# Optimization experiments

Measured on AMD Instinct MI355X. Metric: run time of the kernel, lower is better.

Reference implementation:

```python
import jax, jax.numpy as jnp
import numpy as np

T, B, H = 1024, 4096, 4  # time steps, students, BKT params (l,f,g,s)


def setup_inputs() -> dict:
    key = jax.random.key(0)
    ks = jax.random.split(key, 6)
    # binary correctness sequences, like the original BKT data
    x = (jax.random.uniform(ks[0], (T, B, 1)) < 0.5).astype(jnp.float32)
    y = (jax.random.uniform(ks[1], (T, B, 1)) < 0.5).astype(jnp.float32)
    s = 1.0 / np.sqrt(H)  # torch nn.RNN default init: U(-1/sqrt(H), 1/sqrt(H))
    W_ih = jax.random.uniform(ks[2], (H, 1), minval=-s, maxval=s, dtype=jnp.float32)
    W_hh = jax.random.uniform(ks[3], (H, H), minval=-s, maxval=s, dtype=jnp.float32)
    b_ih = jax.random.uniform(ks[4], (H,), minval=-s, maxval=s, dtype=jnp.float32)
    b_hh = jax.random.uniform(ks[5], (H,), minval=-s, maxval=s, dtype=jnp.float32)
    prior = jnp.array([0.1], dtype=jnp.float32)
    return {"x": x, "y": y, "prior": prior, "W_ih": W_ih, "W_hh": W_hh,
            "b_ih": b_ih, "b_hh": b_hh}


def _bce(p, y):
    # torch BCELoss clamps log terms at -100
    logp = jnp.maximum(jnp.log(p), -100.0)
    log1mp = jnp.maximum(jnp.log(1.0 - p), -100.0)
    return -(y * logp + (1.0 - y) * log1mp).mean()


def _forward(x, y, prior, W_ih, W_hh, b_ih, b_hh):
    Bn = x.shape[1]
    Hn = W_hh.shape[0]

    # --- Elman RNN (tanh), seq-first, h0 = 0 ---
    def rnn_step(h, x_t):  # x_t: [B,1], h: [B,H]
        h = jnp.tanh(x_t @ W_ih.T + b_ih + h @ W_hh.T + b_hh)
        return h, h

    h0 = jnp.zeros((Bn, Hn), dtype=x.dtype)
    _, output = jax.lax.scan(rnn_step, h0, x)  # [T,B,H]
    params = (output + 1.0) / 2.0  # map tanh output into (0,1)

    # --- sequential nonlinear BKT latent recurrence ---
    latent0 = jnp.broadcast_to(jax.nn.sigmoid(prior), (Bn, 1)).astype(x.dtype)

    def bkt_step(latent, inp):
        p_t, y_t = inp  # p_t: [B,H], y_t: [B,1]
        l, f, g, s = p_t[:, 0:1], p_t[:, 1:2], p_t[:, 2:3], p_t[:, 3:4]
        correct = latent * (1 - s) + (1 - latent) * g
        k_t1 = latent * (1 - s) / (latent * (1 - s) + (1 - latent) * g)
        k_t0 = latent * s / (latent * s + (1 - latent) * (1 - g))
        m_t = k_t1 * correct + k_t0 * (1 - correct)
        next_latent = m_t * (1 - f) + (1 - m_t) * l
        return next_latent, (correct, next_latent, _bce(correct, y_t))

    _, (corrects, latents, losses) = jax.lax.scan(bkt_step, latent0, (params, y))
    loss = losses.mean()  # sum of per-step BCE / T
    return corrects, latents, loss


def reference(x, y, prior, W_ih, W_hh, b_ih, b_hh):
    return _forward(x, y, prior, W_ih, W_hh, b_ih, b_hh)
```

## Files before the change

kernel.cpp:

```cpp
#include <hip/hip_runtime.h>

#define TT 1024
#define BB 4096
#define CHUNK 64
#define WARM 160
#define NCH (TT / CHUNK)
#define NWMAX 7

typedef float v2f __attribute__((ext_vector_type(2)));

__launch_bounds__(64, 1)
__global__ void bkt_rnn_k(const float* __restrict__ x,
                          const float* __restrict__ y,
                          const float* __restrict__ prior,
                          const float* __restrict__ W_ih,
                          const float* __restrict__ W_hh,
                          const float* __restrict__ b_ih,
                          const float* __restrict__ b_hh,
                          float* __restrict__ out,
                          float* __restrict__ lossPart)
{
    __shared__ unsigned xls[NWMAX * 64];

    const int lane = threadIdx.x;
    const int c  = blockIdx.x >> 6;
    const int eg = blockIdx.x & 63;
    const int e  = eg * 64 + lane;

    const int t_out0  = c * CHUNK;
    const int nwarm   = (t_out0 > WARM) ? WARM : t_out0;
    const int t_start = t_out0 - nwarm;
    const int nww     = nwarm >> 5;
    const int nwords  = nww + 2;

    const float* xp = x + (size_t)t_start * BB + e;
    for (int wd = 0; wd < nwords; ++wd) {
        unsigned m = 0;
        #pragma unroll
        for (int i = 0; i < 32; ++i)
            if (xp[(size_t)(wd * 32 + i) * BB] != 0.0f) m |= (1u << i);
        xls[wd * 64 + lane] = m;
    }
    const float* ypb = y + (size_t)t_out0 * BB + e;
    unsigned yw0 = 0, yw1 = 0;
    #pragma unroll
    for (int i = 0; i < 32; ++i) {
        if (ypb[(size_t)i * BB] != 0.0f)        yw0 |= (1u << i);
        if (ypb[(size_t)(i + 32) * BB] != 0.0f) yw1 |= (1u << i);
    }

    const float S = 2.8853900817779268f;
    float basev[4], swv[4], vv[4][4];
    #pragma unroll
    for (int jj = 0; jj < 4; ++jj) {
        float rowsum = W_hh[jj * 4 + 0] + W_hh[jj * 4 + 1] + W_hh[jj * 4 + 2] + W_hh[jj * 4 + 3];
        basev[jj] = S * (b_ih[jj] + b_hh[jj] + rowsum);
        swv[jj]   = S * W_ih[jj];
        #pragma unroll
        for (int kk = 0; kk < 4; ++kk) vv[jj][kk] = -2.f * S * W_hh[jj * 4 + kk];
    }
    const v2f base01 = {basev[0], basev[1]}, base23 = {basev[2], basev[3]};
    const v2f sw01   = {swv[0],   swv[1]},   sw23   = {swv[2],   swv[3]};
    const v2f c0_01 = {vv[0][0], vv[1][0]}, c0_23 = {vv[2][0], vv[3][0]};
    const v2f c1_01 = {vv[0][1], vv[1][1]}, c1_23 = {vv[2][1], vv[3][1]};
    const v2f c2_01 = {vv[0][2], vv[1][2]}, c2_23 = {vv[2][2], vv[3][2]};
    const v2f c3_01 = {vv[0][3], vv[1][3]}, c3_23 = {vv[2][3], vv[3][3]};

    float lat = 1.0f / (1.0f + __builtin_amdgcn_exp2f(-1.4426950408889634f * prior[0]));
    float r0 = 0.5f, r1 = 0.5f, r2 = 0.5f, r3 = 0.5f;
    float lossAcc = 0.0f;

    auto step = [&](float xf) {
        v2f xv  = {xf, xf};
        v2f r0b = {r0, r0}, r1b = {r1, r1}, r2b = {r2, r2}, r3b = {r3, r3};
        v2f z01 = __builtin_elementwise_fma(xv, sw01, base01);
        v2f z23 = __builtin_elementwise_fma(xv, sw23, base23);
        z01 = __builtin_elementwise_fma(r0b, c0_01, z01);
        z23 = __builtin_elementwise_fma(r0b, c0_23, z23);
        z01 = __builtin_elementwise_fma(r1b, c1_01, z01);
        z23 = __builtin_elementwise_fma(r1b, c1_23, z23);
        z01 = __builtin_elementwise_fma(r2b, c2_01, z01);
        z23 = __builtin_elementwise_fma(r2b, c2_23, z23);
        z01 = __builtin_elementwise_fma(r3b, c3_01, z01);
        z23 = __builtin_elementwise_fma(r3b, c3_23, z23);
        r0 = __builtin_amdgcn_rcpf(__builtin_amdgcn_exp2f(z01.x) + 1.0f);
        r1 = __builtin_amdgcn_rcpf(__builtin_amdgcn_exp2f(z01.y) + 1.0f);
        r2 = __builtin_amdgcn_rcpf(__builtin_amdgcn_exp2f(z23.x) + 1.0f);
        r3 = __builtin_amdgcn_rcpf(__builtin_amdgcn_exp2f(z23.y) + 1.0f);
    };

    for (int wd = 0; wd < nww; ++wd) {
        unsigned m = xls[wd * 64 + lane];
        #pragma unroll 8
        for (int i = 0; i < 32; ++i) {
            step((float)((m >> i) & 1u));
            lat = fmaf(lat, (r0 + r1) - 1.0f, 1.0f - r0);
        }
    }

    unsigned mo0 = xls[nww * 64 + lane];
    unsigned mo1 = xls[(nww + 1) * 64 + lane];
    float* cO = out + (size_t)t_out0 * BB + e;
    float* lO = cO + (size_t)TT * BB;

    auto outblock = [&](unsigned mw, unsigned yw, int tb) {
        float prod = 1.0f;
        #pragma unroll 8
        for (int i = 0; i < 32; ++i) {
            step((float)((mw >> i) & 1u));
            float corr = fmaf(lat, (r2 + r3) - 1.0f, 1.0f - r2);
            float nl   = fmaf(lat, (r0 + r1) - 1.0f, 1.0f - r0);
            const size_t off = (size_t)(tb + i) * BB;
            cO[off] = corr;
            lO[off] = nl;
            float lp = ((yw >> i) & 1u) ? corr : (1.0f - corr);
            prod *= lp;
            if ((i & 7) == 7) {
                lossAcc += __builtin_amdgcn_logf(prod) * 0.6931471805599453f;
                prod = 1.0f;
            }
            lat = nl;
        }
    };
    outblock(mo0, yw0, 0);
    outblock(mo1, yw1, 32);

    #pragma unroll
    for (int o = 32; o >= 1; o >>= 1) lossAcc += __shfl_xor(lossAcc, o, 64);
    if (lane == 0) lossPart[blockIdx.x] = lossAcc;
}

__global__ void reduce_k(const float* __restrict__ part, float* __restrict__ loss) {
    float acc = 0.f;
    for (int i = threadIdx.x; i < 1024; i += 256) acc += part[i];
    #pragma unroll
    for (int o = 32; o >= 1; o >>= 1) acc += __shfl_xor(acc, o, 64);
    __shared__ float w[4];
    if ((threadIdx.x & 63) == 0) w[threadIdx.x >> 6] = acc;
    __syncthreads();
    if (threadIdx.x == 0) {
        float t = w[0] + w[1] + w[2] + w[3];
        *loss = t * (-1.0f / ((float)TT * (float)BB));
    }
}

extern "C" void kernel_launch(void* const* d_in, const int* in_sizes, int n_in,
                              void* d_out, int out_size, void* d_ws, size_t ws_size,
                              hipStream_t stream) {
    const float* x    = (const float*)d_in[0];
    const float* y    = (const float*)d_in[1];
    const float* pr   = (const float*)d_in[2];
    const float* W_ih = (const float*)d_in[3];
    const float* W_hh = (const float*)d_in[4];
    const float* b_ih = (const float*)d_in[5];
    const float* b_hh = (const float*)d_in[6];
    float* out = (float*)d_out;
    float* lossPart = (float*)d_ws;

    bkt_rnn_k<<<NCH * 64, 64, 0, stream>>>(x, y, pr, W_ih, W_hh, b_ih, b_hh, out, lossPart);
    reduce_k<<<1, 256, 0, stream>>>(lossPart, out + 2 * (size_t)TT * BB);
}
```

Baseline: 117.6 us.

## Split BKT recurrence into affine chunk scan with shorter RNN warmup

```diff
diff --git a/kernel.cpp b/kernel.cpp
--- a/kernel.cpp
+++ b/kernel.cpp
@@ -3,111 +3,216 @@
 #define TT 1024
 #define BB 4096
 #define CHUNK 64
-#define WARM 160
+#define WH 64
 #define NCH (TT / CHUNK)
-#define NWMAX 7
+#define NB  (NCH * BB)
+
+#define WS_A   1024
+#define WS_B   (WS_A + NB)
+#define WS_H   (WS_B + NB)
+#define WS_XW  (WS_H + 4 * NB)
 
 typedef float v2f __attribute__((ext_vector_type(2)));
 
+struct StepC {
+    v2f base01, base23, sw01, sw23;
+    v2f c0_01, c0_23, c1_01, c1_23, c2_01, c2_23, c3_01, c3_23;
+};
+
+__device__ __forceinline__ StepC make_consts(const float* W_ih, const float* W_hh,
+                                             const float* b_ih, const float* b_hh) {
+    const float S = 2.8853900817779268f;
+    float basev[4], swv[4], vv[4][4];
+    #pragma unroll
+    for (int jj = 0; jj < 4; ++jj) {
+        float rowsum = W_hh[jj*4+0] + W_hh[jj*4+1] + W_hh[jj*4+2] + W_hh[jj*4+3];
+        basev[jj] = S * (b_ih[jj] + b_hh[jj] + rowsum);
+        swv[jj]   = S * W_ih[jj];
+        #pragma unroll
+        for (int kk = 0; kk < 4; ++kk) vv[jj][kk] = -2.f * S * W_hh[jj*4+kk];
+    }
+    StepC K;
+    K.base01 = {basev[0], basev[1]}; K.base23 = {basev[2], basev[3]};
+    K.sw01   = {swv[0],   swv[1]};   K.sw23   = {swv[2],   swv[3]};
+    K.c0_01 = {vv[0][0], vv[1][0]};  K.c0_23 = {vv[2][0], vv[3][0]};
+    K.c1_01 = {vv[0][1], vv[1][1]};  K.c1_23 = {vv[2][1], vv[3][1]};
+    K.c2_01 = {vv[0][2], vv[1][2]};  K.c2_23 = {vv[2][2], vv[3][2]};
+    K.c3_01 = {vv[0][3], vv[1][3]};  K.c3_23 = {vv[2][3], vv[3][3]};
+    return K;
+}
+
+__device__ __forceinline__ void rnn_step(const StepC& K, float xf,
+                                         float& r0, float& r1, float& r2, float& r3) {
+    v2f xv  = {xf, xf};
+    v2f r0b = {r0, r0}, r1b = {r1, r1}, r2b = {r2, r2}, r3b = {r3, r3};
+    v2f z01 = __builtin_elementwise_fma(xv, K.sw01, K.base01);
+    v2f z23 = __builtin_elementwise_fma(xv, K.sw23, K.base23);
+    z01 = __builtin_elementwise_fma(r0b, K.c0_01, z01);
+    z23 = __builtin_elementwise_fma(r0b, K.c0_23, z23);
+    z01 = __builtin_elementwise_fma(r1b, K.c1_01, z01);
+    z23 = __builtin_elementwise_fma(r1b, K.c1_23, z23);
+    z01 = __builtin_elementwise_fma(r2b, K.c2_01, z01);
+    z23 = __builtin_elementwise_fma(r2b, K.c2_23, z23);
+    z01 = __builtin_elementwise_fma(r3b, K.c3_01, z01);
+    z23 = __builtin_elementwise_fma(r3b, K.c3_23, z23);
+    r0 = __builtin_amdgcn_rcpf(__builtin_amdgcn_exp2f(z01.x) + 1.0f);
+    r1 = __builtin_amdgcn_rcpf(__builtin_amdgcn_exp2f(z01.y) + 1.0f);
+    r2 = __builtin_amdgcn_rcpf(__builtin_amdgcn_exp2f(z23.x) + 1.0f);
+    r3 = __builtin_amdgcn_rcpf(__builtin_amdgcn_exp2f(z23.y) + 1.0f);
+}
+
 __launch_bounds__(64, 1)
-__global__ void bkt_rnn_k(const float* __restrict__ x,
-                          const float* __restrict__ y,
-                          const float* __restrict__ prior,
-                          const float* __restrict__ W_ih,
-                          const float* __restrict__ W_hh,
-                          const float* __restrict__ b_ih,
-                          const float* __restrict__ b_hh,
-                          float* __restrict__ out,
-                          float* __restrict__ lossPart)
+__global__ void bkt_pass1(const float* __restrict__ x,
+                          const float* __restrict__ W_ih, const float* __restrict__ W_hh,
+                          const float* __restrict__ b_ih, const float* __restrict__ b_hh,
+                          float* __restrict__ ws)
 {
-    __shared__ unsigned xls[NWMAX * 64];
-
     const int lane = threadIdx.x;
     const int c  = blockIdx.x >> 6;
     const int eg = blockIdx.x & 63;
     const int e  = eg * 64 + lane;
-
-    const int t_out0  = c * CHUNK;
-    const int nwarm   = (t_out0 > WARM) ? WARM : t_out0;
-    const int t_start = t_out0 - nwarm;
-    const int nww     = nwarm >> 5;
-    const int nwords  = nww + 2;
-
+    const int t0 = c * CHUNK;
+    const int t_start = (c == 0) ? 0 : (t0 - WH);
     const float* xp = x + (size_t)t_start * BB + e;
-    for (int wd = 0; wd < nwords; ++wd) {
+
+    float bufA[32], bufB[32];
+    auto issueA = [&](int wd) {
+        const float* p = xp + (size_t)wd * 32 * BB;
+        #pragma unroll
+        for (int i = 0; i < 32; ++i) bufA[i] = p[(size_t)i * BB];
+    };
+    auto issueB = [&](int wd) {
+        const float* p = xp + (size_t)wd * 32 * BB;
+        #pragma unroll
+        for (int i = 0; i < 32; ++i) bufB[i] = p[(size_t)i * BB];
+    };
+    auto packA = [&]() -> unsigned {
         unsigned m = 0;
         #pragma unroll
+        for (int i = 0; i < 32; ++i) if (bufA[i] != 0.0f) m |= (1u << i);
+        return m;
+    };
+    auto packB = [&]() -> unsigned {
+        unsigned m = 0;
+        #pragma unroll
+        for (int i = 0; i < 32; ++i) if (bufB[i] != 0.0f) m |= (1u << i);
+        return m;
+    };
+
+    const StepC K = make_consts(W_ih, W_hh, b_ih, b_hh);
+    float r0 = 0.5f, r1 = 0.5f, r2 = 0.5f, r3 = 0.5f;
+
+    auto run32_warm = [&](unsigned m) {
+        #pragma unroll 8
         for (int i = 0; i < 32; ++i)
-            if (xp[(size_t)(wd * 32 + i) * BB] != 0.0f) m |= (1u << i);
-        xls[wd * 64 + lane] = m;
-    }
-    const float* ypb = y + (size_t)t_out0 * BB + e;
-    unsigned yw0 = 0, yw1 = 0;
-    #pragma unroll
-    for (int i = 0; i < 32; ++i) {
-        if (ypb[(size_t)i * BB] != 0.0f)        yw0 |= (1u << i);
-        if (ypb[(size_t)(i + 32) * BB] != 0.0f) yw1 |= (1u << i);
-    }
-
-    const float S = 2.8853900817779268f;
-    float basev[4], swv[4], vv[4][4];
-    #pragma unroll
-    for (int jj = 0; jj < 4; ++jj) {
-        float rowsum = W_hh[jj * 4 + 0] + W_hh[jj * 4 + 1] + W_hh[jj * 4 + 2] + W_hh[jj * 4 + 3];
-        basev[jj] = S * (b_ih[jj] + b_hh[jj] + rowsum);
-        swv[jj]   = S * W_ih[jj];
-        #pragma unroll
-        for (int kk = 0; kk < 4; ++kk) vv[jj][kk] = -2.f * S * W_hh[jj * 4 + kk];
-    }
-    const v2f base01 = {basev[0], basev[1]}, base23 = {basev[2], basev[3]};
-    const v2f sw01   = {swv[0],   swv[1]},   sw23   = {swv[2],   swv[3]};
-    const v2f c0_01 = {vv[0][0], vv[1][0]}, c0_23 = {vv[2][0], vv[3][0]};
-    const v2f c1_01 = {vv[0][1], vv[1][1]}, c1_23 = {vv[2][1], vv[3][1]};
-    const v2f c2_01 = {vv[0][2], vv[1][2]}, c2_23 = {vv[2][2], vv[3][2]};
-    const v2f c3_01 = {vv[0][3], vv[1][3]}, c3_23 = {vv[2][3], vv[3][3]};
-
-    float lat = 1.0f / (1.0f + __builtin_amdgcn_exp2f(-1.4426950408889634f * prior[0]));
-    float r0 = 0.5f, r1 = 0.5f, r2 = 0.5f, r3 = 0.5f;
-    float lossAcc = 0.0f;
-
-    auto step = [&](float xf) {
-        v2f xv  = {xf, xf};
-        v2f r0b = {r0, r0}, r1b = {r1, r1}, r2b = {r2, r2}, r3b = {r3, r3};
-        v2f z01 = __builtin_elementwise_fma(xv, sw01, base01);
-        v2f z23 = __builtin_elementwise_fma(xv, sw23, base23);
-        z01 = __builtin_elementwise_fma(r0b, c0_01, z01);
-        z23 = __builtin_elementwise_fma(r0b, c0_23, z23);
-        z01 = __builtin_elementwise_fma(r1b, c1_01, z01);
-        z23 = __builtin_elementwise_fma(r1b, c1_23, z23);
-        z01 = __builtin_elementwise_fma(r2b, c2_01, z01);
-        z23 = __builtin_elementwise_fma(r2b, c2_23, z23);
-        z01 = __builtin_elementwise_fma(r3b, c3_01, z01);
-        z23 = __builtin_elementwise_fma(r3b, c3_23, z23);
-        r0 = __builtin_amdgcn_rcpf(__builtin_amdgcn_exp2f(z01.x) + 1.0f);
-        r1 = __builtin_amdgcn_rcpf(__builtin_amdgcn_exp2f(z01.y) + 1.0f);
-        r2 = __builtin_amdgcn_rcpf(__builtin_amdgcn_exp2f(z23.x) + 1.0f);
-        r3 = __builtin_amdgcn_rcpf(__builtin_amdgcn_exp2f(z23.y) + 1.0f);
-    };
-
-    for (int wd = 0; wd < nww; ++wd) {
-        unsigned m = xls[wd * 64 + lane];
+            rnn_step(K, (float)((m >> i) & 1u), r0, r1, r2, r3);
+    };
+
+    float A = 1.0f, Bacc = 0.0f;
+    auto run32_acc = [&](unsigned m) {
         #pragma unroll 8
         for (int i = 0; i < 32; ++i) {
-            step((float)((m >> i) & 1u));
-            lat = fmaf(lat, (r0 + r1) - 1.0f, 1.0f - r0);
+            rnn_step(K, (float)((m >> i) & 1u), r0, r1, r2, r3);
+            float a = (r0 + r1) - 1.0f;
+            Bacc = fmaf(a, Bacc, 1.0f - r0);
+            A *= a;
         }
-    }
-
-    unsigned mo0 = xls[nww * 64 + lane];
-    unsigned mo1 = xls[(nww + 1) * 64 + lane];
-    float* cO = out + (size_t)t_out0 * BB + e;
+    };
+
+    float s0, s1, s2, s3;
+    unsigned mo0, mo1;
+
+    if (c == 0) {
+        issueA(0); issueB(1);
+        s0 = s1 = s2 = s3 = 0.5f;
+        mo0 = packA();
+        run32_acc(mo0);
+        mo1 = packB();
+        run32_acc(mo1);
+    } else {
+        issueA(0); issueB(1);
+        unsigned mw0 = packA();
+        issueA(2);
+        run32_warm(mw0);
+        unsigned mw1 = packB();
+        issueB(3);
+        run32_warm(mw1);
+        s0 = r0; s1 = r1; s2 = r2; s3 = r3;
+        mo0 = packA();
+        run32_acc(mo0);
+        mo1 = packB();
+        run32_acc(mo1);
+    }
+
+    const int idx = c * BB + e;
+    ws[WS_A + idx] = A;
+    ws[WS_B + idx] = Bacc;
+    ws[WS_H + 0 * NB + idx] = s0;
+    ws[WS_H + 1 * NB + idx] = s1;
+    ws[WS_H + 2 * NB + idx] = s2;
+    ws[WS_H + 3 * NB + idx] = s3;
+    unsigned* wsu = (unsigned*)ws;
+    wsu[WS_XW + 0 * NB + idx] = mo0;
+    wsu[WS_XW + 1 * NB + idx] = mo1;
+}
+
+__launch_bounds__(64, 1)
+__global__ void bkt_pass2(const float* __restrict__ y, const float* __restrict__ prior,
+                          const float* __restrict__ W_ih, const float* __restrict__ W_hh,
+                          const float* __restrict__ b_ih, const float* __restrict__ b_hh,
+                          float* __restrict__ out, float* __restrict__ ws)
+{
+    const int lane = threadIdx.x;
+    const int c  = blockIdx.x >> 6;
+    const int eg = blockIdx.x & 63;
+    const int e  = eg * 64 + lane;
+    const int t0 = c * CHUNK;
+    const int idx = c * BB + e;
+
+    float Av[NCH - 1], Bv[NCH - 1];
+    #pragma unroll
+    for (int cc = 0; cc < NCH - 1; ++cc) {
+        Av[cc] = ws[WS_A + cc * BB + e];
+        Bv[cc] = ws[WS_B + cc * BB + e];
+    }
+    float r0 = ws[WS_H + 0 * NB + idx];
+    float r1 = ws[WS_H + 1 * NB + idx];
+    float r2 = ws[WS_H + 2 * NB + idx];
+    float r3 = ws[WS_H + 3 * NB + idx];
+    const unsigned* wsu = (const unsigned*)ws;
+    unsigned mo0 = wsu[WS_XW + 0 * NB + idx];
+    unsigned mo1 = wsu[WS_XW + 1 * NB + idx];
+
+    const float* ypb = y + (size_t)t0 * BB + e;
+    float yA[32], yB[32];
+    #pragma unroll
+    for (int i = 0; i < 32; ++i) yA[i] = ypb[(size_t)i * BB];
+    #pragma unroll
+    for (int i = 0; i < 32; ++i) yB[i] = ypb[(size_t)(i + 32) * BB];
+
+    const StepC K = make_consts(W_ih, W_hh, b_ih, b_hh);
+
+    float lat = 1.0f / (1.0f + __builtin_amdgcn_exp2f(-1.4426950408889634f * prior[0]));
+    #pragma unroll
+    for (int cc = 0; cc < NCH - 1; ++cc)
+        lat = (cc < c) ? fmaf(Av[cc], lat, Bv[cc]) : lat;
+
+    unsigned yw0 = 0, yw1 = 0;
+    #pragma unroll
+    for (int i = 0; i < 32; ++i) {
+        if (yA[i] != 0.0f) yw0 |= (1u << i);
+        if (yB[i] != 0.0f) yw1 |= (1u << i);
+    }
+
+    float* cO = out + (size_t)t0 * BB + e;
     float* lO = cO + (size_t)TT * BB;
+    float lossAcc = 0.0f;
 
     auto outblock = [&](unsigned mw, unsigned yw, int tb) {
         float prod = 1.0f;
         #pragma unroll 8
         for (int i = 0; i < 32; ++i) {
-            step((float)((mw >> i) & 1u));
+            rnn_step(K, (float)((mw >> i) & 1u), r0, r1, r2, r3);
             float corr = fmaf(lat, (r2 + r3) - 1.0f, 1.0f - r2);
             float nl   = fmaf(lat, (r0 + r1) - 1.0f, 1.0f - r0);
             const size_t off = (size_t)(tb + i) * BB;
@@ -127,7 +232,7 @@
 
     #pragma unroll
     for (int o = 32; o >= 1; o >>= 1) lossAcc += __shfl_xor(lossAcc, o, 64);
-    if (lane == 0) lossPart[blockIdx.x] = lossAcc;
+    if (lane == 0) ws[blockIdx.x] = lossAcc;
 }
 
 __global__ void reduce_k(const float* __restrict__ part, float* __restrict__ loss) {
@@ -155,8 +260,9 @@
     const float* b_ih = (const float*)d_in[5];
     const float* b_hh = (const float*)d_in[6];
     float* out = (float*)d_out;
-    float* lossPart = (float*)d_ws;
-
-    bkt_rnn_k<<<NCH * 64, 64, 0, stream>>>(x, y, pr, W_ih, W_hh, b_ih, b_hh, out, lossPart);
-    reduce_k<<<1, 256, 0, stream>>>(lossPart, out + 2 * (size_t)TT * BB);
-}
+    float* ws  = (float*)d_ws;
+
+    bkt_pass1<<<NCH * 64, 64, 0, stream>>>(x, W_ih, W_hh, b_ih, b_hh, ws);
+    bkt_pass2<<<NCH * 64, 64, 0, stream>>>(y, pr, W_ih, W_hh, b_ih, b_hh, out, ws);
+    reduce_k<<<1, 256, 0, stream>>>(ws, out + 2 * (size_t)TT * BB);
+}
```

New measurement: 115.7 us. About the same (-1.6%).
